# Performance work log

Measured on AMD Instinct MI355X. Metric: run time of the kernel, lower is better.

## Reference

```python
import math
import jax, jax.numpy as jnp
import numpy as np

N_LAYERS = 6
N_HEADS = 8
WINDOW = 4
LN_EPS = 1e-6


def _get_rel_emb(emb, length):
    # emb: [1, 2*WINDOW+1, kc] -> [1, 2*length-1, kc]
    max_rel = 2 * WINDOW + 1
    pad = max(0, length - (WINDOW + 1))
    start = max(0, WINDOW + 1 - length)
    end = max_rel + 2 * length - 1
    if pad > 0:
        emb = jnp.pad(emb, ((0, 0), (pad, pad), (0, 0)))
    return emb[:, start:end]


def _rel_to_abs(x):
    # x: [b,h,l,2l-1] -> [b,h,l,l]
    b, h, l, _ = x.shape
    x = jnp.pad(x, ((0, 0), (0, 0), (0, 0), (0, 1)))
    xf = x.reshape(b, h, l * 2 * l)
    xf = jnp.pad(xf, ((0, 0), (0, 0), (0, l - 1)))
    return xf.reshape(b, h, l + 1, 2 * l - 1)[:, :, :l, l - 1:]


def _abs_to_rel(x):
    # x: [b,h,l,l] -> [b,h,l,2l-1]
    b, h, l, _ = x.shape
    x = jnp.pad(x, ((0, 0), (0, 0), (0, 0), (0, l - 1)))
    xf = x.reshape(b, h, -1)
    xf = jnp.pad(xf, ((0, 0), (0, 0), (l, 0)))
    return xf.reshape(b, h, l, 2 * l)[..., 1:]


def _layer_norm(x, scale, bias):
    m = jnp.mean(x, axis=-1, keepdims=True)
    v = jnp.mean(jnp.square(x - m), axis=-1, keepdims=True)
    return (x - m) * jax.lax.rsqrt(v + LN_EPS) * scale + bias


def _forward(x, x_mask, Wq, bq, Wk, bk, Wv, bv, Wo, bo, emb_rel_k, emb_rel_v,
             ln1_scale, ln1_bias, W1, b1, W2, b2, ln2_scale, ln2_bias):
    B, T, C = x.shape
    H = N_HEADS
    KC = C // H
    scale = 1.0 / math.sqrt(KC)
    attn_mask = x_mask[:, :, None, :] * x_mask[:, :, :, None]  # [B,1,T,T]
    mask_t = jnp.transpose(x_mask, (0, 2, 1))  # [B,T,1]
    x = x * mask_t
    for l in range(N_LAYERS):
        # --- relative-position multi-head self-attention ---
        q = (x @ Wq[l] + bq[l]).reshape(B, T, H, KC).transpose(0, 2, 1, 3)
        k = (x @ Wk[l] + bk[l]).reshape(B, T, H, KC).transpose(0, 2, 1, 3)
        v = (x @ Wv[l] + bv[l]).reshape(B, T, H, KC).transpose(0, 2, 1, 3)
        scores = jnp.einsum('bhqd,bhkd->bhqk', q * scale, k)
        rk = _get_rel_emb(emb_rel_k[l], T)[0]  # [2T-1, KC] (heads shared)
        rel_logits = jnp.einsum('bhld,md->bhlm', q * scale, rk)
        scores = scores + _rel_to_abs(rel_logits)
        scores = jnp.where(attn_mask == 0, -10000.0, scores)
        p = jax.nn.softmax(scores, axis=-1)
        out = jnp.einsum('bhqk,bhkd->bhqd', p, v)
        rv = _get_rel_emb(emb_rel_v[l], T)[0]
        out = out + jnp.einsum('bhlm,md->bhld', _abs_to_rel(p), rv)
        out = out.transpose(0, 2, 1, 3).reshape(B, T, C)
        y = out @ Wo[l] + bo[l]
        x = _layer_norm(x + y, ln1_scale[l], ln1_bias[l])
        # --- pointwise conv FFN (kernel_size=1) ---
        h1 = jax.nn.relu((x * mask_t) @ W1[l] + b1[l])
        y = (h1 * mask_t) @ W2[l] + b2[l]
        y = y * mask_t
        x = _layer_norm(x + y, ln2_scale[l], ln2_bias[l])
    return x * mask_t


def setup_inputs() -> dict:
    key = jax.random.key(0)
    B, T, C, F, L, H = 8, 768, 512, 2048, N_LAYERS, N_HEADS
    KC = C // H
    ks = jax.random.split(key, 10)
    nrm = lambda k, s, sd=0.02: jax.random.normal(k, s, jnp.float32) * sd
    return {
        'x': jax.random.normal(ks[0], (B, T, C), jnp.float32),
        'x_mask': jnp.ones((B, 1, T), jnp.float32),
        'Wq': nrm(ks[1], (L, C, C)), 'bq': jnp.zeros((L, C), jnp.float32),
        'Wk': nrm(ks[2], (L, C, C)), 'bk': jnp.zeros((L, C), jnp.float32),
        'Wv': nrm(ks[3], (L, C, C)), 'bv': jnp.zeros((L, C), jnp.float32),
        'Wo': nrm(ks[4], (L, C, C)), 'bo': jnp.zeros((L, C), jnp.float32),
        'emb_rel_k': nrm(ks[5], (L, 1, 2 * WINDOW + 1, KC), KC ** -0.5),
        'emb_rel_v': nrm(ks[6], (L, 1, 2 * WINDOW + 1, KC), KC ** -0.5),
        'ln1_scale': jnp.ones((L, C), jnp.float32), 'ln1_bias': jnp.zeros((L, C), jnp.float32),
        'W1': nrm(ks[7], (L, C, F)), 'b1': jnp.zeros((L, F), jnp.float32),
        'W2': nrm(ks[8], (L, F, C)), 'b2': jnp.zeros((L, C), jnp.float32),
        'ln2_scale': jnp.ones((L, C), jnp.float32), 'ln2_bias': jnp.zeros((L, C), jnp.float32),
    }


def reference(x, x_mask, Wq, bq, Wk, bk, Wv, bv, Wo, bo, emb_rel_k, emb_rel_v,
              ln1_scale, ln1_bias, W1, b1, W2, b2, ln2_scale, ln2_bias):
    return _forward(x, x_mask, Wq, bq, Wk, bk, Wv, bv, Wo, bo, emb_rel_k, emb_rel_v,
                    ln1_scale, ln1_bias, W1, b1, W2, b2, ln2_scale, ln2_bias)
```

## Files before the change

kernel.cpp:

```cpp
#include <hip/hip_runtime.h>
#include <stdint.h>


typedef unsigned short u16;
typedef __attribute__((ext_vector_type(8))) __bf16 bf16x8;
typedef __attribute__((ext_vector_type(4))) float f32x4;

#define B_ 8
#define T_ 768
#define C_ 512
#define F_ 2048

__device__ __forceinline__ float b2f(u16 u) {
    union { float f; uint32_t i; } x; x.i = ((uint32_t)u) << 16; return x.f;
}
__device__ __forceinline__ u16 f2b(float f) {
    union { float f; uint32_t i; } x; x.f = f;
    return (u16)((x.i + 0x7fffu + ((x.i >> 16) & 1u)) >> 16);
}

template <int TN, int EPI>
__global__ __launch_bounds__(128 * (TN / 64)) void gemm_bt(
    const u16* __restrict__ A, long long aB1, long long aB2, int aStride,
    const u16* __restrict__ Bt, long long bB1, long long bB2, int bStride,
    const float* __restrict__ bias,
    u16* __restrict__ out, long long oB1, long long oB2, int oStride,
    int K, float epiScale)
{
    constexpr int WN = TN / 64;
    constexpr int NT = 128 * WN;
    const int tid = threadIdx.x;
    const int wave = tid >> 6, lane = tid & 63;
    const int wm = wave & 1, wn = wave >> 1;
    const int quad = lane >> 4, l16 = lane & 15;
    const int zb = blockIdx.z >> 3, zh = blockIdx.z & 7;
    A   += (long long)zb * aB1 + (long long)zh * aB2;
    Bt  += (long long)zb * bB1 + (long long)zh * bB2;
    out += (long long)zb * oB1 + (long long)zh * oB2;
    const int m0 = blockIdx.x * 128;
    const int n0 = blockIdx.y * TN;

    __shared__ u16 As[128 * 64];
    __shared__ u16 Bs[TN * 64];

    const f32x4 vzero = {0.f, 0.f, 0.f, 0.f};
    f32x4 acc[4][4];
#pragma unroll
    for (int i = 0; i < 4; ++i)
#pragma unroll
        for (int j = 0; j < 4; ++j) acc[i][j] = vzero;

    for (int k0 = 0; k0 < K; k0 += 64) {
#pragma unroll
        for (int i = 0; i < 1024 / NT; ++i) {
            int c = tid + i * NT;
            int row = c >> 3, pc = c & 7, lc = pc ^ (row & 7);
            *(uint4*)&As[c * 8] =
                *(const uint4*)(A + (long long)(m0 + row) * aStride + (k0 + lc * 8));
        }
#pragma unroll
        for (int i = 0; i < (TN * 8) / NT; ++i) {
            int c = tid + i * NT;
            int row = c >> 3, pc = c & 7, lc = pc ^ (row & 7);
            *(uint4*)&Bs[c * 8] =
                *(const uint4*)(Bt + (long long)(n0 + row) * bStride + (k0 + lc * 8));
        }
        __syncthreads();
#pragma unroll
        for (int ks = 0; ks < 2; ++ks) {
            bf16x8 af[4], bfr[4];
#pragma unroll
            for (int mi = 0; mi < 4; ++mi) {
                int row = wm * 64 + mi * 16 + l16;
                int pc = ((ks << 2) | quad) ^ (row & 7);
                af[mi] = *(const bf16x8*)&As[row * 64 + pc * 8];
            }
#pragma unroll
            for (int ni = 0; ni < 4; ++ni) {
                int row = wn * 64 + ni * 16 + l16;
                int pc = ((ks << 2) | quad) ^ (row & 7);
                bfr[ni] = *(const bf16x8*)&Bs[row * 64 + pc * 8];
            }
#pragma unroll
            for (int mi = 0; mi < 4; ++mi)
#pragma unroll
                for (int ni = 0; ni < 4; ++ni)
                    acc[mi][ni] = __builtin_amdgcn_mfma_f32_16x16x32_bf16(
                        bfr[ni], af[mi], acc[mi][ni], 0, 0, 0);
        }
        __syncthreads();
    }

#pragma unroll
    for (int mi = 0; mi < 4; ++mi) {
        int row = m0 + wm * 64 + mi * 16 + l16;
#pragma unroll
        for (int ni = 0; ni < 4; ++ni) {
            int colb = n0 + wn * 64 + ni * 16 + quad * 4;
            u16 pk[4];
#pragma unroll
            for (int r = 0; r < 4; ++r) {
                float v = acc[mi][ni][r] + (bias ? bias[colb + r] : 0.f);
                if (EPI == 1) v = v > 0.f ? v : 0.f;
                if (EPI == 3) { if (colb + r < 512) v *= epiScale; }
                pk[r] = f2b(v);
            }
            uint2 p;
            p.x = (uint32_t)pk[0] | ((uint32_t)pk[1] << 16);
            p.y = (uint32_t)pk[2] | ((uint32_t)pk[3] << 16);
            *(uint2*)(out + (long long)row * oStride + colb) = p;
        }
    }
}

__global__ __launch_bounds__(256) void bandg_k(
    const u16* __restrict__ qkv, const float* __restrict__ erk,
    float* __restrict__ bandg)
{
    __shared__ float erkS[576];
    const int tid = threadIdx.x;
    for (int idx = tid; idx < 576; idx += 256) erkS[idx] = erk[idx];
    __syncthreads();
    const int gid = blockIdx.x * 256 + tid;
    const int row = gid >> 3, h = gid & 7;
    const u16* q = qkv + (long long)row * 1536 + h * 64;
    float acc[9];
#pragma unroll
    for (int e = 0; e < 9; ++e) acc[e] = 0.f;
#pragma unroll
    for (int c = 0; c < 8; ++c) {
        uint4 d4 = *(const uint4*)(q + c * 8);
        const uint32_t dw[4] = {d4.x, d4.y, d4.z, d4.w};
#pragma unroll
        for (int j = 0; j < 8; ++j) {
            u16 uu = (u16)((dw[j >> 1] >> ((j & 1) * 16)) & 0xffff);
            float qv = b2f(uu);
            int d = c * 8 + j;
#pragma unroll
            for (int e = 0; e < 9; ++e) acc[e] += qv * erkS[e * 64 + d];
        }
    }
    float* o = bandg + (long long)gid * 9;
#pragma unroll
    for (int e = 0; e < 9; ++e) o[e] = acc[e];
}

__global__ __launch_bounds__(256) void flash_attn(
    const u16* __restrict__ qkv, const u16* __restrict__ vt,
    const float* __restrict__ mask, const float* __restrict__ bandg,
    const float* __restrict__ erv, u16* __restrict__ outb)
{
    const int tid = threadIdx.x;
    const int w = tid >> 6, lane = tid & 63;
    const int quad = lane >> 4, l16 = lane & 15;
    const int qt = blockIdx.x, bh = blockIdx.y, b = bh >> 3, h = bh & 7;
    const int q0 = qt * 64;

    __shared__ u16 Ql[64 * 64];
    __shared__ u16 Kt[64 * 64];
    __shared__ u16 Vt[64 * 64];
    __shared__ u16 Pl[4][16 * 64];
    __shared__ float bandk[64][10];
    __shared__ float maskK[64];

#pragma unroll
    for (int i = 0; i < 2; ++i) {
        int c = tid + i * 256;
        int r = c >> 3, pc = c & 7, lc = pc ^ (r & 7);
        *(uint4*)&Ql[c * 8] =
            *(const uint4*)(qkv + (long long)(b * T_ + q0 + r) * 1536 + h * 64 + lc * 8);
    }
    for (int idx = tid; idx < 576; idx += 256) {
        int r = idx / 9, e = idx - r * 9;
        bandk[r][e] = bandg[((long long)(b * T_ + q0 + r) * 8 + h) * 9 + e];
    }

    const int i_row = q0 + w * 16 + l16;
    const float mi = mask[b * T_ + i_row];
    float m_run = -1e30f, l_run = 0.f;
    const f32x4 vzero = {0.f, 0.f, 0.f, 0.f};
    f32x4 vacc[4] = {vzero, vzero, vzero, vzero};
    float pb[3] = {0.f, 0.f, 0.f};

    __syncthreads();
    bf16x8 qf[2];
#pragma unroll
    for (int ks = 0; ks < 2; ++ks) {
        int r = w * 16 + l16;
        int pc = ((ks << 2) | quad) ^ (r & 7);
        qf[ks] = *(const bf16x8*)&Ql[r * 64 + pc * 8];
    }

    for (int kt = 0; kt < 12; ++kt) {
        __syncthreads();
#pragma unroll
        for (int i = 0; i < 2; ++i) {
            int c = tid + i * 256;
            int r = c >> 3, pc = c & 7, lc = pc ^ (r & 7);
            *(uint4*)&Kt[c * 8] =
                *(const uint4*)(qkv + (long long)(b * T_ + kt * 64 + r) * 1536 + 512 + h * 64 + lc * 8);
        }
#pragma unroll
        for (int i = 0; i < 2; ++i) {
            int c = tid + i * 256;
            int r = c >> 3, pc = c & 7, lc = pc ^ (r & 7);
            *(uint4*)&Vt[c * 8] =
                *(const uint4*)(vt + ((long long)bh * 64 + r) * T_ + kt * 64 + lc * 8);
        }
        if (tid < 64) maskK[tid] = mask[b * T_ + kt * 64 + tid];
        __syncthreads();

        f32x4 sacc[4];
#pragma unroll
        for (int ni = 0; ni < 4; ++ni) sacc[ni] = vzero;
#pragma unroll
        for (int ks = 0; ks < 2; ++ks)
#pragma unroll
            for (int ni = 0; ni < 4; ++ni) {
                int r = ni * 16 + l16;
                int pc = ((ks << 2) | quad) ^ (r & 7);
                bf16x8 kf = *(const bf16x8*)&Kt[r * 64 + pc * 8];
                sacc[ni] = __builtin_amdgcn_mfma_f32_16x16x32_bf16(kf, qf[ks], sacc[ni], 0, 0, 0);
            }

        float mx = -1e30f;
#pragma unroll
        for (int ni = 0; ni < 4; ++ni)
#pragma unroll
            for (int r = 0; r < 4; ++r) {
                int jl = ni * 16 + quad * 4 + r;
                int j = kt * 64 + jl;
                float s = sacc[ni][r];
                int dlt = j - i_row;
                if (dlt >= -4 && dlt <= 4) s += bandk[w * 16 + l16][dlt + 4];
                if (mi * maskK[jl] == 0.f) s = -10000.0f;
                sacc[ni][r] = s;
                mx = fmaxf(mx, s);
            }
        mx = fmaxf(mx, __shfl_xor(mx, 16));
        mx = fmaxf(mx, __shfl_xor(mx, 32));
        float m_new = fmaxf(m_run, mx);
        float alpha = __expf(m_run - m_new);
        m_run = m_new;
        l_run *= alpha;
#pragma unroll
        for (int ni = 0; ni < 4; ++ni) vacc[ni] = vacc[ni] * alpha;
#pragma unroll
        for (int k = 0; k < 3; ++k) pb[k] *= alpha;

        float lsum = 0.f;
#pragma unroll
        for (int ni = 0; ni < 4; ++ni) {
            u16 pk[4];
#pragma unroll
            for (int r = 0; r < 4; ++r) {
                float u = __expf(sacc[ni][r] - m_new);
                lsum += u;
                pk[r] = f2b(u);
            }
            int c0 = ni * 16 + quad * 4;
            int phys = (((c0 >> 3) ^ (l16 & 7)) << 3) + (c0 & 7);
            uint2 p;
            p.x = (uint32_t)pk[0] | ((uint32_t)pk[1] << 16);
            p.y = (uint32_t)pk[2] | ((uint32_t)pk[3] << 16);
            *(uint2*)&Pl[w][l16 * 64 + phys] = p;
        }
        l_run += lsum;

#pragma unroll
        for (int k = 0; k < 3; ++k) {
            int e = quad * 3 + k;
            if (e < 9) {
                int jl = i_row + e - 4 - kt * 64;
                if (jl >= 0 && jl < 64) {
                    int phys = (((jl >> 3) ^ (l16 & 7)) << 3) + (jl & 7);
                    pb[k] += b2f(Pl[w][l16 * 64 + phys]);
                }
            }
        }

#pragma unroll
        for (int ks = 0; ks < 2; ++ks) {
            int pcc = ((ks << 2) | quad) ^ (l16 & 7);
            bf16x8 pf = *(const bf16x8*)&Pl[w][l16 * 64 + pcc * 8];
#pragma unroll
            for (int ni = 0; ni < 4; ++ni) {
                int r = ni * 16 + l16;
                int pc = ((ks << 2) | quad) ^ (r & 7);
                bf16x8 vf = *(const bf16x8*)&Vt[r * 64 + pc * 8];
                vacc[ni] = __builtin_amdgcn_mfma_f32_16x16x32_bf16(vf, pf, vacc[ni], 0, 0, 0);
            }
        }
    }

    l_run += __shfl_xor(l_run, 16);
    l_run += __shfl_xor(l_run, 32);
    const float rinv = 1.f / l_run;

    float pband[9];
#pragma unroll
    for (int e = 0; e < 9; ++e) {
        float val = (quad == e / 3) ? pb[e % 3] : 0.f;
        val += __shfl_xor(val, 16);
        val += __shfl_xor(val, 32);
        pband[e] = val * rinv;
    }

    u16* orow = outb + (long long)(b * T_ + i_row) * C_ + h * 64;
#pragma unroll
    for (int ni = 0; ni < 4; ++ni) {
        u16 pk[4];
#pragma unroll
        for (int r = 0; r < 4; ++r) {
            int d = ni * 16 + quad * 4 + r;
            float v = vacc[ni][r] * rinv;
#pragma unroll
            for (int e = 0; e < 9; ++e) v += pband[e] * erv[e * 64 + d];
            pk[r] = f2b(v);
        }
        uint2 p;
        p.x = (uint32_t)pk[0] | ((uint32_t)pk[1] << 16);
        p.y = (uint32_t)pk[2] | ((uint32_t)pk[3] << 16);
        *(uint2*)(orow + ni * 16 + quad * 4) = p;
    }
}

__global__ void transpose_qkvo(const float* __restrict__ Wq, const float* __restrict__ Wk,
                               const float* __restrict__ Wv, const float* __restrict__ Wo,
                               u16* __restrict__ wqkvT, u16* __restrict__ woT)
{
    __shared__ u16 tile[32][33];
    const int z = blockIdx.z, l = z >> 2, which = z & 3;
    const float* src = (which == 0 ? Wq : which == 1 ? Wk : which == 2 ? Wv : Wo)
                       + (long long)l * 262144;
    u16* dst = (which == 3) ? woT + (long long)l * 262144
                            : wqkvT + (long long)l * 786432 + which * 262144;
    const int r0 = blockIdx.y * 32, c0 = blockIdx.x * 32;
    const int tx = threadIdx.x, ty = threadIdx.y;
#pragma unroll
    for (int i = 0; i < 32; i += 8)
        tile[ty + i][tx] = f2b(src[(long long)(r0 + ty + i) * 512 + (c0 + tx)]);
    __syncthreads();
#pragma unroll
    for (int i = 0; i < 32; i += 8)
        dst[(long long)(c0 + ty + i) * 512 + (r0 + tx)] = tile[tx][ty + i];
}

__global__ void transpose_f2bL(const float* __restrict__ src0, int sStride, long long sLayer,
                               u16* __restrict__ dst0, int dStride, long long dLayer)
{
    __shared__ u16 tile[32][33];
    const int l = blockIdx.z;
    const float* src = src0 + (long long)l * sLayer;
    u16* dst = dst0 + (long long)l * dLayer;
    const int r0 = blockIdx.y * 32, c0 = blockIdx.x * 32;
    const int tx = threadIdx.x, ty = threadIdx.y;
#pragma unroll
    for (int i = 0; i < 32; i += 8)
        tile[ty + i][tx] = f2b(src[(long long)(r0 + ty + i) * sStride + (c0 + tx)]);
    __syncthreads();
#pragma unroll
    for (int i = 0; i < 32; i += 8)
        dst[(long long)(c0 + ty + i) * dStride + (r0 + tx)] = tile[tx][ty + i];
}

__global__ void transpose_b(const u16* __restrict__ src, long long sB1, long long sB2, int sStride,
                            u16* __restrict__ dst, long long dB1, long long dB2, int dStride)
{
    __shared__ u16 tile[32][33];
    const int z = blockIdx.z, zb = z >> 3, zh = z & 7;
    src += (long long)zb * sB1 + (long long)zh * sB2;
    dst += (long long)zb * dB1 + (long long)zh * dB2;
    const int r0 = blockIdx.y * 32, c0 = blockIdx.x * 32;
    const int tx = threadIdx.x, ty = threadIdx.y;
#pragma unroll
    for (int i = 0; i < 32; i += 8)
        tile[ty + i][tx] = src[(long long)(r0 + ty + i) * sStride + (c0 + tx)];
    __syncthreads();
#pragma unroll
    for (int i = 0; i < 32; i += 8)
        dst[(long long)(c0 + ty + i) * dStride + (r0 + tx)] = tile[tx][ty + i];
}

__global__ void concat_bias(const float* __restrict__ bq, const float* __restrict__ bk,
                            const float* __restrict__ bv, float* __restrict__ dst)
{
    int i = blockIdx.x * 256 + threadIdx.x;
    int l = i / 1536, n = i - l * 1536;
    float v = (n < 512) ? bq[l * 512 + n]
             : (n < 1024 ? bk[l * 512 + (n - 512)] : bv[l * 512 + (n - 1024)]);
    dst[i] = v;
}

__global__ void mask_in(const float* __restrict__ x, const float* __restrict__ mask,
                        u16* __restrict__ out)
{
    int i4 = (blockIdx.x * 256 + threadIdx.x) * 4;
    float4 xv = *(const float4*)(x + i4);
    float m = mask[i4 >> 9];
    u16 pk[4] = {f2b(xv.x * m), f2b(xv.y * m), f2b(xv.z * m), f2b(xv.w * m)};
    uint2 p; p.x = (uint32_t)pk[0] | ((uint32_t)pk[1] << 16);
    p.y = (uint32_t)pk[2] | ((uint32_t)pk[3] << 16);
    *(uint2*)(out + i4) = p;
}

__global__ void mask_out(const u16* __restrict__ x, const float* __restrict__ mask,
                         float* __restrict__ out)
{
    int i4 = (blockIdx.x * 256 + threadIdx.x) * 4;
    uint2 p = *(const uint2*)(x + i4);
    float m = mask[i4 >> 9];
    float4 o;
    o.x = b2f((u16)(p.x & 0xffff)) * m;
    o.y = b2f((u16)(p.x >> 16)) * m;
    o.z = b2f((u16)(p.y & 0xffff)) * m;
    o.w = b2f((u16)(p.y >> 16)) * m;
    *(float4*)(out + i4) = o;
}

__global__ __launch_bounds__(256) void add_ln(
    const u16* __restrict__ x, const u16* __restrict__ y,
    const float* __restrict__ sc, const float* __restrict__ bi,
    u16* __restrict__ outx)
{
    const int wave = threadIdx.x >> 6, lane = threadIdx.x & 63;
    const long long r = (long long)blockIdx.x * 4 + wave;
    const u16* xr = x + r * C_;
    const u16* yr = y + r * C_;
    float v[8], s = 0.f;
#pragma unroll
    for (int it = 0; it < 2; ++it) {
        int j0 = it * 256 + lane * 4;
        uint2 px = *(const uint2*)(xr + j0);
        uint2 py = *(const uint2*)(yr + j0);
        v[it * 4 + 0] = b2f((u16)(px.x & 0xffff)) + b2f((u16)(py.x & 0xffff));
        v[it * 4 + 1] = b2f((u16)(px.x >> 16))    + b2f((u16)(py.x >> 16));
        v[it * 4 + 2] = b2f((u16)(px.y & 0xffff)) + b2f((u16)(py.y & 0xffff));
        v[it * 4 + 3] = b2f((u16)(px.y >> 16))    + b2f((u16)(py.y >> 16));
        s += v[it * 4 + 0] + v[it * 4 + 1] + v[it * 4 + 2] + v[it * 4 + 3];
    }
#pragma unroll
    for (int off = 32; off > 0; off >>= 1) s += __shfl_down(s, off);
    s = __shfl(s, 0);
    const float mean = s * (1.f / 512.f);
    float var = 0.f;
#pragma unroll
    for (int l = 0; l < 8; ++l) { float d = v[l] - mean; var += d * d; }
#pragma unroll
    for (int off = 32; off > 0; off >>= 1) var += __shfl_down(var, off);
    var = __shfl(var, 0);
    const float rs = rsqrtf(var * (1.f / 512.f) + 1e-6f);
    u16* orow = outx + r * C_;
#pragma unroll
    for (int it = 0; it < 2; ++it) {
        int j0 = it * 256 + lane * 4;
        float4 s4 = *(const float4*)(sc + j0);
        float4 b4 = *(const float4*)(bi + j0);
        u16 pk[4];
        pk[0] = f2b((v[it * 4 + 0] - mean) * rs * s4.x + b4.x);
        pk[1] = f2b((v[it * 4 + 1] - mean) * rs * s4.y + b4.y);
        pk[2] = f2b((v[it * 4 + 2] - mean) * rs * s4.z + b4.z);
        pk[3] = f2b((v[it * 4 + 3] - mean) * rs * s4.w + b4.w);
        uint2 p; p.x = (uint32_t)pk[0] | ((uint32_t)pk[1] << 16);
        p.y = (uint32_t)pk[2] | ((uint32_t)pk[3] << 16);
        *(uint2*)(orow + j0) = p;
    }
}

extern "C" void kernel_launch(void* const* d_in, const int* in_sizes, int n_in,
                              void* d_out, int out_size, void* d_ws, size_t ws_size,
                              hipStream_t stream)
{
    const float* x    = (const float*)d_in[0];
    const float* mask = (const float*)d_in[1];
    const float* Wq   = (const float*)d_in[2];
    const float* bq   = (const float*)d_in[3];
    const float* Wk   = (const float*)d_in[4];
    const float* bk   = (const float*)d_in[5];
    const float* Wv   = (const float*)d_in[6];
    const float* bv   = (const float*)d_in[7];
    const float* Wo   = (const float*)d_in[8];
    const float* bo   = (const float*)d_in[9];
    const float* erk  = (const float*)d_in[10];
    const float* erv  = (const float*)d_in[11];
    const float* ln1s = (const float*)d_in[12];
    const float* ln1b = (const float*)d_in[13];
    const float* W1   = (const float*)d_in[14];
    const float* b1   = (const float*)d_in[15];
    const float* W2   = (const float*)d_in[16];
    const float* b2   = (const float*)d_in[17];
    const float* ln2s = (const float*)d_in[18];
    const float* ln2b = (const float*)d_in[19];
    float* out = (float*)d_out;
    u16* ws  = (u16*)d_ws;

    const long long CF = 512LL * 2048;
    const int M = B_ * T_;

    u16* wqkvT   = ws;
    u16* woT     = ws + 4718592;
    u16* w1T     = ws + 6291456;
    u16* w2T     = ws + 12582912;
    float* bqkv  = (float*)(ws + 18874368);
    u16* xb      = ws + 18892800;
    u16* qkvb    = ws + 22038528;
    u16* vtb     = ws + 31475712;
    u16* attnb   = ws + 34621440;
    u16* scr     = ws + 37767168;
    float* bandg = (float*)(ws + 50350080);
    u16* yb      = vtb;

    const dim3 tb(32, 8);

    transpose_qkvo<<<dim3(16, 16, 24), tb, 0, stream>>>(Wq, Wk, Wv, Wo, wqkvT, woT);
    transpose_f2bL<<<dim3(64, 16, 6), tb, 0, stream>>>(W1, 2048, CF, w1T, 512, 1048576);
    transpose_f2bL<<<dim3(16, 64, 6), tb, 0, stream>>>(W2, 512,  CF, w2T, 2048, 1048576);
    concat_bias<<<36, 256, 0, stream>>>(bq, bk, bv, bqkv);
    mask_in<<<(M * 512) / 1024, 256, 0, stream>>>(x, mask, xb);

    for (int l = 0; l < 6; ++l) {
        gemm_bt<128, 3><<<dim3(48, 12, 1), 256, 0, stream>>>(
            xb, 0, 0, 512, wqkvT + (long long)l * 786432, 0, 0, 512, bqkv + l * 1536,
            qkvb, 0, 0, 1536, 512, 0.125f);
        bandg_k<<<192, 256, 0, stream>>>(qkvb, erk + l * 576, bandg);
        transpose_b<<<dim3(2, 24, 64), tb, 0, stream>>>(
            qkvb + 1024, 768LL * 1536, 64, 1536,
            vtb, 8LL * 64 * 768, 64LL * 768, 768);
        flash_attn<<<dim3(12, 64), 256, 0, stream>>>(
            qkvb, vtb, mask, bandg, erv + l * 576, attnb);
        gemm_bt<64, 0><<<dim3(48, 8, 1), 128, 0, stream>>>(
            attnb, 0, 0, 512, woT + (long long)l * 262144, 0, 0, 512, bo + l * 512,
            yb, 0, 0, 512, 512, 0.f);
        add_ln<<<1536, 256, 0, stream>>>(xb, yb, ln1s + l * 512, ln1b + l * 512, xb);
        gemm_bt<128, 1><<<dim3(48, 16, 1), 256, 0, stream>>>(
            xb, 0, 0, 512, w1T + (long long)l * 1048576, 0, 0, 512, b1 + l * 2048,
            scr, 0, 0, 2048, 512, 0.f);
        gemm_bt<64, 0><<<dim3(48, 8, 1), 128, 0, stream>>>(
            scr, 0, 0, 2048, w2T + (long long)l * 1048576, 0, 0, 2048, b2 + l * 512,
            yb, 0, 0, 512, 2048, 0.f);
        add_ln<<<1536, 256, 0, stream>>>(xb, yb, ln2s + l * 512, ln2b + l * 512, xb);
    }

    mask_out<<<(M * 512) / 1024, 256, 0, stream>>>(xb, mask, out);
}
```

Before: 1.174 ms.

## Double-buffer K/V tiles in flash attention with register prefetch and band skipping

Restructures the flash-attention key loop to prefetch the next K/V/mask tile into registers while the current tile is computed, then store it to a second shared-memory buffer, so each iteration needs one barrier instead of two. It also remaps block indices so neighbouring blocks hit different heads, skips relative-band bias work on tiles that cannot contain the band, skips masking when the whole tile is unmasked, and raises wave priority around MFMA sections. The cost is more shared memory and more registers held across the loop, which may reduce occupancy.

```diff
diff --git a/kernel.cpp b/kernel.cpp
--- a/kernel.cpp
+++ b/kernel.cpp
@@ -153,15 +153,18 @@
     const int tid = threadIdx.x;
     const int w = tid >> 6, lane = tid & 63;
     const int quad = lane >> 4, l16 = lane & 15;
-    const int qt = blockIdx.x, bh = blockIdx.y, b = bh >> 3, h = bh & 7;
+    const int orig = blockIdx.y * 12 + blockIdx.x;
+    const int swz = (orig & 7) * 96 + (orig >> 3);
+    const int qt = swz % 12, bh = swz / 12;
+    const int b = bh >> 3, h = bh & 7;
     const int q0 = qt * 64;
 
     __shared__ u16 Ql[64 * 64];
-    __shared__ u16 Kt[64 * 64];
-    __shared__ u16 Vt[64 * 64];
+    __shared__ u16 Kt[2][64 * 64];
+    __shared__ u16 Vt[2][64 * 64];
     __shared__ u16 Pl[4][16 * 64];
     __shared__ float bandk[64][10];
-    __shared__ float maskK[64];
+    __shared__ float maskK[2][64];
 
 #pragma unroll
     for (int i = 0; i < 2; ++i) {
@@ -170,6 +173,16 @@
         *(uint4*)&Ql[c * 8] =
             *(const uint4*)(qkv + (long long)(b * T_ + q0 + r) * 1536 + h * 64 + lc * 8);
     }
+#pragma unroll
+    for (int i = 0; i < 2; ++i) {
+        int c = tid + i * 256;
+        int r = c >> 3, pc = c & 7, lc = pc ^ (r & 7);
+        *(uint4*)&Kt[0][c * 8] =
+            *(const uint4*)(qkv + (long long)(b * T_ + r) * 1536 + 512 + h * 64 + lc * 8);
+        *(uint4*)&Vt[0][c * 8] =
+            *(const uint4*)(vt + ((long long)bh * 64 + r) * T_ + lc * 8);
+    }
+    if (tid < 64) maskK[0][tid] = mask[b * T_ + tid];
     for (int idx = tid; idx < 576; idx += 256) {
         int r = idx / 9, e = idx - r * 9;
         bandk[r][e] = bandg[((long long)(b * T_ + q0 + r) * 8 + h) * 9 + e];
@@ -191,52 +204,72 @@
         qf[ks] = *(const bf16x8*)&Ql[r * 64 + pc * 8];
     }
 
+    int cbuf = 0;
     for (int kt = 0; kt < 12; ++kt) {
-        __syncthreads();
-#pragma unroll
-        for (int i = 0; i < 2; ++i) {
-            int c = tid + i * 256;
-            int r = c >> 3, pc = c & 7, lc = pc ^ (r & 7);
-            *(uint4*)&Kt[c * 8] =
-                *(const uint4*)(qkv + (long long)(b * T_ + kt * 64 + r) * 1536 + 512 + h * 64 + lc * 8);
-        }
-#pragma unroll
-        for (int i = 0; i < 2; ++i) {
-            int c = tid + i * 256;
-            int r = c >> 3, pc = c & 7, lc = pc ^ (r & 7);
-            *(uint4*)&Vt[c * 8] =
-                *(const uint4*)(vt + ((long long)bh * 64 + r) * T_ + kt * 64 + lc * 8);
-        }
-        if (tid < 64) maskK[tid] = mask[b * T_ + kt * 64 + tid];
-        __syncthreads();
+        uint4 kreg[2], vreg[2];
+        float mreg = 0.f;
+        const bool pre = (kt < 11);
+        if (pre) {
+            const int ktn = kt + 1;
+#pragma unroll
+            for (int i = 0; i < 2; ++i) {
+                int c = tid + i * 256;
+                int r = c >> 3, pc = c & 7, lc = pc ^ (r & 7);
+                kreg[i] = *(const uint4*)(qkv + (long long)(b * T_ + ktn * 64 + r) * 1536
+                                          + 512 + h * 64 + lc * 8);
+                vreg[i] = *(const uint4*)(vt + ((long long)bh * 64 + r) * T_
+                                          + ktn * 64 + lc * 8);
+            }
+            if (tid < 64) mreg = mask[b * T_ + ktn * 64 + tid];
+        }
+
+        const float mkv = maskK[cbuf][lane];
+        const bool tile_clean = (__ballot(mkv == 0.f) == 0ull);
+        const bool fast = tile_clean && (mi != 0.f);
+        const bool has_band = (kt * 64 <= q0 + w * 16 + 19) &&
+                              (kt * 64 + 67 >= q0 + w * 16);
 
         f32x4 sacc[4];
 #pragma unroll
         for (int ni = 0; ni < 4; ++ni) sacc[ni] = vzero;
+        __builtin_amdgcn_s_setprio(1);
 #pragma unroll
         for (int ks = 0; ks < 2; ++ks)
 #pragma unroll
             for (int ni = 0; ni < 4; ++ni) {
                 int r = ni * 16 + l16;
                 int pc = ((ks << 2) | quad) ^ (r & 7);
-                bf16x8 kf = *(const bf16x8*)&Kt[r * 64 + pc * 8];
+                bf16x8 kf = *(const bf16x8*)&Kt[cbuf][r * 64 + pc * 8];
                 sacc[ni] = __builtin_amdgcn_mfma_f32_16x16x32_bf16(kf, qf[ks], sacc[ni], 0, 0, 0);
             }
+        __builtin_amdgcn_s_setprio(0);
+
+        if (has_band) {
+#pragma unroll
+            for (int ni = 0; ni < 4; ++ni)
+#pragma unroll
+                for (int r = 0; r < 4; ++r) {
+                    int jl = ni * 16 + quad * 4 + r;
+                    int dlt = kt * 64 + jl - i_row;
+                    if (dlt >= -4 && dlt <= 4)
+                        sacc[ni][r] += bandk[w * 16 + l16][dlt + 4];
+                }
+        }
+        if (!fast) {
+#pragma unroll
+            for (int ni = 0; ni < 4; ++ni)
+#pragma unroll
+                for (int r = 0; r < 4; ++r) {
+                    int jl = ni * 16 + quad * 4 + r;
+                    if (mi * maskK[cbuf][jl] == 0.f) sacc[ni][r] = -10000.0f;
+                }
+        }
 
         float mx = -1e30f;
 #pragma unroll
         for (int ni = 0; ni < 4; ++ni)
 #pragma unroll
-            for (int r = 0; r < 4; ++r) {
-                int jl = ni * 16 + quad * 4 + r;
-                int j = kt * 64 + jl;
-                float s = sacc[ni][r];
-                int dlt = j - i_row;
-                if (dlt >= -4 && dlt <= 4) s += bandk[w * 16 + l16][dlt + 4];
-                if (mi * maskK[jl] == 0.f) s = -10000.0f;
-                sacc[ni][r] = s;
-                mx = fmaxf(mx, s);
-            }
+            for (int r = 0; r < 4; ++r) mx = fmaxf(mx, sacc[ni][r]);
         mx = fmaxf(mx, __shfl_xor(mx, 16));
         mx = fmaxf(mx, __shfl_xor(mx, 32));
         float m_new = fmaxf(m_run, mx);
@@ -267,18 +300,21 @@
         }
         l_run += lsum;
 
-#pragma unroll
-        for (int k = 0; k < 3; ++k) {
-            int e = quad * 3 + k;
-            if (e < 9) {
-                int jl = i_row + e - 4 - kt * 64;
-                if (jl >= 0 && jl < 64) {
-                    int phys = (((jl >> 3) ^ (l16 & 7)) << 3) + (jl & 7);
-                    pb[k] += b2f(Pl[w][l16 * 64 + phys]);
+        if (has_band) {
+#pragma unroll
+            for (int k = 0; k < 3; ++k) {
+                int e = quad * 3 + k;
+                if (e < 9) {
+                    int jl = i_row + e - 4 - kt * 64;
+                    if (jl >= 0 && jl < 64) {
+                        int phys = (((jl >> 3) ^ (l16 & 7)) << 3) + (jl & 7);
+                        pb[k] += b2f(Pl[w][l16 * 64 + phys]);
+                    }
                 }
             }
         }
 
+        __builtin_amdgcn_s_setprio(1);
 #pragma unroll
         for (int ks = 0; ks < 2; ++ks) {
             int pcc = ((ks << 2) | quad) ^ (l16 & 7);
@@ -287,9 +323,22 @@
             for (int ni = 0; ni < 4; ++ni) {
                 int r = ni * 16 + l16;
                 int pc = ((ks << 2) | quad) ^ (r & 7);
-                bf16x8 vf = *(const bf16x8*)&Vt[r * 64 + pc * 8];
+                bf16x8 vf = *(const bf16x8*)&Vt[cbuf][r * 64 + pc * 8];
                 vacc[ni] = __builtin_amdgcn_mfma_f32_16x16x32_bf16(vf, pf, vacc[ni], 0, 0, 0);
             }
+        }
+        __builtin_amdgcn_s_setprio(0);
+
+        if (pre) {
+#pragma unroll
+            for (int i = 0; i < 2; ++i) {
+                int c = tid + i * 256;
+                *(uint4*)&Kt[cbuf ^ 1][c * 8] = kreg[i];
+                *(uint4*)&Vt[cbuf ^ 1][c * 8] = vreg[i];
+            }
+            if (tid < 64) maskK[cbuf ^ 1][tid] = mreg;
+            __syncthreads();
+            cbuf ^= 1;
         }
     }
 
```

After: 1.125 ms. 1.04x faster.
